# Performance work log

Hardware: AMD Instinct MI355X
Metric: run time of the kernel (lower is better)

The kernel has to match this reference:

```python
import jax, jax.numpy as jnp
import numpy as np

H = 12
D_MODEL = 768
H_D = D_MODEL // H


def setup_inputs() -> dict:
    key = jax.random.key(0)
    ks = jax.random.split(key, 11)
    B, S = 2, 2048
    scale_in = 1.0
    w_scale = 1.0 / np.sqrt(D_MODEL)
    inp = {
        "query": jax.random.normal(ks[0], (B, S, D_MODEL), dtype=jnp.float32),
        "key": jax.random.normal(ks[1], (B, S, D_MODEL), dtype=jnp.float32),
        "value": jax.random.normal(ks[2], (B, S, D_MODEL), dtype=jnp.float32),
        "wq": jax.random.normal(ks[3], (D_MODEL, D_MODEL), dtype=jnp.float32) * w_scale,
        "bq": jnp.zeros((D_MODEL,), dtype=jnp.float32),
        "wk": jax.random.normal(ks[4], (D_MODEL, D_MODEL), dtype=jnp.float32) * w_scale,
        "bk": jnp.zeros((D_MODEL,), dtype=jnp.float32),
        "wv": jax.random.normal(ks[5], (D_MODEL, D_MODEL), dtype=jnp.float32) * w_scale,
        "bv": jnp.zeros((D_MODEL,), dtype=jnp.float32),
        "wo": jax.random.normal(ks[6], (D_MODEL, D_MODEL), dtype=jnp.float32) * w_scale,
        "bo": jnp.zeros((D_MODEL,), dtype=jnp.float32),
    }
    return inp


def reference(query, key, value, wq, bq, wk, bk, wv, bv, wo, bo):
    B, S, _ = query.shape
    # QKV projections, split into heads: [B, H, S, h_d]
    def proj(x, w, b):
        y = jnp.einsum("bsd,de->bse", x, w) + b
        return y.reshape(B, S, H, H_D).transpose(0, 2, 1, 3)

    q = proj(query, wq, bq)
    k = proj(key, wk, bk)
    v = proj(value, wv, bv)

    # scaled dot-product attention (dropout disabled / eval mode)
    scores = jnp.einsum("bhsd,bhtd->bhst", q, k) / jnp.sqrt(jnp.float32(H_D))
    wm = jax.nn.softmax(scores, axis=-1)  # [B, H, S, S]
    out = jnp.einsum("bhst,bhtd->bhsd", wm, v)

    # merge heads and output projection
    out = out.transpose(0, 2, 1, 3).reshape(B, S, D_MODEL)
    out = jnp.einsum("bsd,de->bse", out, wo) + bo
    return out
```

## Files before the change

kernel.cpp:

```cpp
#include <hip/hip_runtime.h>

#define H 12
#define DM 768
#define HD 64
#define SEQ 2048
#define BATCH 2
#define MROWS (BATCH*SEQ)

typedef __attribute__((ext_vector_type(8))) short short8;
typedef __attribute__((ext_vector_type(4))) float f32x4;
typedef __attribute__((ext_vector_type(16))) float f32x16;
using u16 = unsigned short;
using u32 = unsigned int;

__device__ __forceinline__ float bf2f(u16 u) { return __uint_as_float(((u32)u) << 16); }
__device__ __forceinline__ u16 f2bf(float x) {
  u32 u = __float_as_uint(x);
  return (u16)((u + 0x7fffu + ((u >> 16) & 1u)) >> 16);
}
__device__ __forceinline__ u32 cvt_pk_bf16(float lo, float hi) {
  u32 r;
  asm("v_cvt_pk_bf16_f32 %0, %1, %2" : "=v"(r) : "v"(lo), "v"(hi));
  return r;
}
__device__ __forceinline__ void gl2lds16(const u16* __restrict__ g, u16* l) {
  __builtin_amdgcn_global_load_lds(
      (const __attribute__((address_space(1))) unsigned int*)g,
      (__attribute__((address_space(3))) unsigned int*)l,
      16, 0, 0);
}

#define C_SM 0.18033688011112042f

__global__ __launch_bounds__(256) void transpose_w4(const float* __restrict__ w0, const float* __restrict__ w1,
                                                    const float* __restrict__ w2, const float* __restrict__ w3,
                                                    u16* __restrict__ dst0)
{
  __shared__ u16 Ts[64][72];
  const float* src = blockIdx.z == 0 ? w0 : blockIdx.z == 1 ? w1 : blockIdx.z == 2 ? w2 : w3;
  u16* dst = dst0 + (size_t)blockIdx.z * DM * DM;
  const int t = threadIdx.x;
  const int r0 = blockIdx.y * 64, c0 = blockIdx.x * 64;
  const int row = t >> 2, cq = (t & 3) * 16;
  const float* sp = src + (size_t)(r0 + row) * DM + c0 + cq;
  #pragma unroll
  for (int g = 0; g < 4; ++g) {
    float4 a = *reinterpret_cast<const float4*>(sp + g * 4);
    Ts[row][cq + g * 4 + 0] = f2bf(a.x);
    Ts[row][cq + g * 4 + 1] = f2bf(a.y);
    Ts[row][cq + g * 4 + 2] = f2bf(a.z);
    Ts[row][cq + g * 4 + 3] = f2bf(a.w);
  }
  __syncthreads();
  union { uint4 v[2]; u16 e[16]; } pk;
  #pragma unroll
  for (int j = 0; j < 16; ++j) pk.e[j] = Ts[cq + j][row];
  uint4* dp = reinterpret_cast<uint4*>(dst + (size_t)(c0 + row) * DM + r0 + cq);
  dp[0] = pk.v[0];
  dp[1] = pk.v[1];
}

template<int BM, bool AF32>
__device__ __forceinline__ void gemm_core(const void* __restrict__ Av, const u16* __restrict__ Bt,
                                          const float* __restrict__ bias, void* __restrict__ dstv,
                                          int mode, int bx, int by, float outScale)
{
  constexpr int AFR = BM / 32;
  constexpr int ACH = BM / 32;
  __shared__ u16 As[BM * 64];
  __shared__ u16 Bs[128 * 64];
  const int t = threadIdx.x;
  const int lane = t & 63, w = t >> 6;
  const int l15 = lane & 15, l4 = lane >> 4;
  const int m0 = by * BM, n0 = bx * 128;
  const int wr = (w >> 1) * (BM / 2), wc = (w & 1) * 64;

  f32x4 acc[AFR][4] = {};

  for (int kt = 0; kt < DM / 64; ++kt) {
    const int k0 = kt * 64;
    #pragma unroll
    for (int c = 0; c < ACH; ++c) {
      const int id = c * 256 + t;
      const int row = id >> 3, xc = id & 7;
      const int db = row * 128 + ((xc * 16) ^ ((row & 7) << 4));
      if (AF32) {
        const float* Af = reinterpret_cast<const float*>(Av) + (size_t)(m0 + row) * DM + k0 + xc * 8;
        float4 a0 = *reinterpret_cast<const float4*>(Af);
        float4 a1 = *reinterpret_cast<const float4*>(Af + 4);
        uint4 v;
        v.x = cvt_pk_bf16(a0.x, a0.y);
        v.y = cvt_pk_bf16(a0.z, a0.w);
        v.z = cvt_pk_bf16(a1.x, a1.y);
        v.w = cvt_pk_bf16(a1.z, a1.w);
        *reinterpret_cast<uint4*>(reinterpret_cast<char*>(As) + db) = v;
      } else {
        uint4 va = *reinterpret_cast<const uint4*>(reinterpret_cast<const u16*>(Av) +
                   (size_t)(m0 + row) * DM + k0 + xc * 8);
        *reinterpret_cast<uint4*>(reinterpret_cast<char*>(As) + db) = va;
      }
    }
    #pragma unroll
    for (int c = 0; c < 4; ++c) {
      const int id = c * 256 + t;
      const int row = id >> 3, xc = id & 7;
      const int db = row * 128 + ((xc * 16) ^ ((row & 7) << 4));
      uint4 vb = *reinterpret_cast<const uint4*>(Bt + (size_t)(n0 + row) * DM + k0 + xc * 8);
      *reinterpret_cast<uint4*>(reinterpret_cast<char*>(Bs) + db) = vb;
    }
    __syncthreads();
    #pragma unroll
    for (int ks = 0; ks < 2; ++ks) {
      short8 ag[AFR], bg[4];
      #pragma unroll
      for (int i = 0; i < AFR; ++i) {
        const int ar = wr + i * 16 + l15;
        ag[i] = *reinterpret_cast<const short8*>(reinterpret_cast<const char*>(As) +
                 ar * 128 + ((ks * 64 + l4 * 16) ^ ((ar & 7) << 4)));
      }
      #pragma unroll
      for (int j = 0; j < 4; ++j) {
        const int br = wc + j * 16 + l15;
        bg[j] = *reinterpret_cast<const short8*>(reinterpret_cast<const char*>(Bs) +
                 br * 128 + ((ks * 64 + l4 * 16) ^ ((br & 7) << 4)));
      }
      #pragma unroll
      for (int i = 0; i < AFR; ++i)
        #pragma unroll
        for (int j = 0; j < 4; ++j)
          acc[i][j] = __builtin_amdgcn_mfma_f32_16x16x32_bf16(ag[i], bg[j], acc[i][j], 0, 0, 0);
    }
    __syncthreads();
  }

  #pragma unroll
  for (int j = 0; j < 4; ++j) {
    const int gcol = n0 + wc + j * 16 + l15;
    const float bb = bias[gcol];
    #pragma unroll
    for (int i = 0; i < AFR; ++i) {
      const int grow = m0 + wr + i * 16 + l4 * 4;
      if (mode == 2) {
        float* dst = reinterpret_cast<float*>(dstv);
        #pragma unroll
        for (int r = 0; r < 4; ++r)
          dst[(size_t)(grow + r) * DM + gcol] = acc[i][j][r] + bb;
      } else {
        u16* dst = reinterpret_cast<u16*>(dstv);
        const int b = grow >> 11, s = grow & (SEQ - 1);
        const int h = gcol >> 6, d = gcol & 63;
        if (mode == 0) {
          #pragma unroll
          for (int r = 0; r < 4; ++r)
            dst[((size_t)(b * H + h) * SEQ + s + r) * HD + d] = f2bf((acc[i][j][r] + bb) * outScale);
        } else {
          union { uint2 v; u16 e[4]; } pk;
          #pragma unroll
          for (int r = 0; r < 4; ++r) pk.e[r] = f2bf(acc[i][j][r] + bb);
          *reinterpret_cast<uint2*>(dst + ((size_t)(b * H + h) * HD + d) * SEQ + s) = pk.v;
        }
      }
    }
  }
}

__global__ __launch_bounds__(256) void gemm_qkv_kernel(
    const float* __restrict__ xq, const float* __restrict__ xk, const float* __restrict__ xv,
    const u16* __restrict__ wT, const float* __restrict__ bq, const float* __restrict__ bk,
    const float* __restrict__ bv, u16* __restrict__ Qb, u16* __restrict__ Kb, u16* __restrict__ Vtb)
{
  const int flat = blockIdx.z * 384 + blockIdx.y * 6 + blockIdx.x;
  const int nb = (flat & 7) * 144 + (flat >> 3);
  const int z = nb / 384, rem = nb % 384;
  const int by = rem / 6, bx = rem % 6;
  const float* A    = z == 0 ? xq : z == 1 ? xk : xv;
  const u16* Bt     = wT + (size_t)z * DM * DM;
  const float* bias = z == 0 ? bq : z == 1 ? bk : bv;
  u16* dst          = z == 0 ? Qb : z == 1 ? Kb : Vtb;
  const float sc    = z == 1 ? C_SM : 1.0f;
  gemm_core<64, true>(A, Bt, bias, dst, z == 2 ? 1 : 0, bx, by, sc);
}

__global__ __launch_bounds__(256) void gemm_o_kernel(const u16* __restrict__ A, const u16* __restrict__ woT,
                                                     const float* __restrict__ bo, float* __restrict__ out)
{
  const int flat = blockIdx.y * 6 + blockIdx.x;
  const int nb = (flat & 7) * 96 + (flat >> 3);
  gemm_core<32, false>(A, woT, bo, out, 2, nb % 6, nb / 6, 1.0f);
}

__global__ __launch_bounds__(256) void attn_kernel(const u16* __restrict__ Q, const u16* __restrict__ K,
                                                   const u16* __restrict__ Vt, u16* __restrict__ attn)
{
  __shared__ u16 Ks[2][64 * 64];
  __shared__ u16 Vs[2][64 * 64];
  __shared__ u16 Qs[128 * 64];
  const int t = threadIdx.x;
  const int lane = t & 63, w = t >> 6;
  const int l31 = lane & 31, hi = lane >> 5;
  const int flat = blockIdx.y * 16 + blockIdx.x;
  const int nbid = (flat & 7) * 48 + (flat >> 3);
  const int q0 = (nbid & 15) * 128;
  const int bh = nbid >> 4;
  const size_t qbase  = ((size_t)bh * SEQ + q0) * HD;
  const size_t kbase0 = (size_t)bh * SEQ * HD;
  const size_t vtbase = (size_t)bh * HD * SEQ;

  const int r8 = lane >> 3;
  const int pcol = ((lane & 7) ^ r8) * 8;

  #pragma unroll
  for (int j = 0; j < 4; ++j) {
    const int ci = w * 4 + j;
    gl2lds16(Q + qbase + (size_t)(ci * 8 + r8) * HD + pcol, &Qs[ci * 512]);
  }
  #pragma unroll
  for (int j = 0; j < 2; ++j) {
    const int ci = w * 2 + j;
    const int row = ci * 8 + r8;
    gl2lds16(K + kbase0 + (size_t)row * HD + pcol, &Ks[0][ci * 512]);
    gl2lds16(Vt + vtbase + (size_t)row * SEQ + pcol, &Vs[0][ci * 512]);
  }
  asm volatile("s_waitcnt vmcnt(4)" ::: "memory");

  short8 qf[4];
  {
    const int qr = w * 32 + l31;
    #pragma unroll
    for (int ks = 0; ks < 4; ++ks)
      qf[ks] = *reinterpret_cast<const short8*>(reinterpret_cast<const char*>(Qs) +
               qr * 128 + (((ks * 32 + hi * 16)) ^ ((qr & 7) << 4)));
  }

  f32x16 oacc[2] = {};
  float l_s = 0.f;
  int cur = 0;

  for (int kt = 0; kt < SEQ / 64; ++kt) {
    asm volatile("s_waitcnt vmcnt(0)" ::: "memory");
    __builtin_amdgcn_s_barrier();

    if (kt + 1 < SEQ / 64) {
      const int nxt = cur ^ 1;
      #pragma unroll
      for (int j = 0; j < 2; ++j) {
        const int ci = w * 2 + j;
        const int row = ci * 8 + r8;
        gl2lds16(K + kbase0 + (size_t)((kt + 1) * 64 + row) * HD + pcol, &Ks[nxt][ci * 512]);
        gl2lds16(Vt + vtbase + (size_t)row * SEQ + (kt + 1) * 64 + pcol, &Vs[nxt][ci * 512]);
      }
    }

    f32x16 s0 = {}, s1 = {};
    __builtin_amdgcn_s_setprio(1);
    #pragma unroll
    for (int ks = 0; ks < 4; ++ks) {
      const int cb = ks * 32 + hi * 16;
      short8 kf0 = *reinterpret_cast<const short8*>(reinterpret_cast<const char*>(Ks[cur]) +
                   l31 * 128 + (cb ^ ((l31 & 7) << 4)));
      short8 kf1 = *reinterpret_cast<const short8*>(reinterpret_cast<const char*>(Ks[cur]) +
                   (32 + l31) * 128 + (cb ^ ((l31 & 7) << 4)));
      s0 = __builtin_amdgcn_mfma_f32_32x32x16_bf16(kf0, qf[ks], s0, 0, 0, 0);
      s1 = __builtin_amdgcn_mfma_f32_32x32x16_bf16(kf1, qf[ks], s1, 0, 0, 0);
    }
    __builtin_amdgcn_s_setprio(0);

    float p0[16], p1[16], psum = 0.f;
    #pragma unroll
    for (int r = 0; r < 16; ++r) {
      p0[r] = exp2f(s0[r]);
      p1[r] = exp2f(s1[r]);
      psum += p0[r] + p1[r];
    }
    l_s += psum;

    __builtin_amdgcn_s_setprio(1);
    #pragma unroll
    for (int ks2 = 0; ks2 < 4; ++ks2) {
      const float* P = (ks2 < 2) ? p0 : p1;
      const int ro = (ks2 & 1) * 8;
      u32 a0 = cvt_pk_bf16(P[ro + 0], P[ro + 1]);
      u32 a1 = cvt_pk_bf16(P[ro + 2], P[ro + 3]);
      u32 b0 = cvt_pk_bf16(P[ro + 4], P[ro + 5]);
      u32 b1 = cvt_pk_bf16(P[ro + 6], P[ro + 7]);
      asm volatile("v_permlane32_swap_b32 %0, %1" : "+v"(a0), "+v"(b0));
      asm volatile("v_permlane32_swap_b32 %0, %1" : "+v"(a1), "+v"(b1));
      union { u32 u[4]; short8 s; } pa;
      pa.u[0] = a0; pa.u[1] = a1; pa.u[2] = b0; pa.u[3] = b1;
      const int cb2 = ks2 * 32 + hi * 16;
      #pragma unroll
      for (int dt = 0; dt < 2; ++dt) {
        const int vr = dt * 32 + l31;
        short8 vf = *reinterpret_cast<const short8*>(reinterpret_cast<const char*>(Vs[cur]) +
                    vr * 128 + (cb2 ^ ((vr & 7) << 4)));
        oacc[dt] = __builtin_amdgcn_mfma_f32_32x32x16_bf16(pa.s, vf, oacc[dt], 0, 0, 0);
      }
    }
    __builtin_amdgcn_s_setprio(0);
    cur ^= 1;
  }

  const float l_tot = l_s + __shfl_xor(l_s, 32);
  const int b = bh / H, h = bh % H;
  #pragma unroll
  for (int r = 0; r < 16; ++r) {
    const int qo = (r & 3) + 8 * (r >> 2) + 4 * hi;
    const float inv = 1.f / __shfl(l_tot, qo);
    const int qg = q0 + w * 32 + qo;
    const size_t base = ((size_t)(b * SEQ + qg)) * DM + h * HD;
    attn[base + l31]      = f2bf(oacc[0][r] * inv);
    attn[base + 32 + l31] = f2bf(oacc[1][r] * inv);
  }
}

extern "C" void kernel_launch(void* const* d_in, const int* in_sizes, int n_in,
                              void* d_out, int out_size, void* d_ws, size_t ws_size,
                              hipStream_t stream)
{
  const float* q  = (const float*)d_in[0];
  const float* k  = (const float*)d_in[1];
  const float* v  = (const float*)d_in[2];
  const float* wq = (const float*)d_in[3];
  const float* bq = (const float*)d_in[4];
  const float* wk = (const float*)d_in[5];
  const float* bk = (const float*)d_in[6];
  const float* wv = (const float*)d_in[7];
  const float* bv = (const float*)d_in[8];
  const float* wo = (const float*)d_in[9];
  const float* bo = (const float*)d_in[10];

  u16* ws = (u16*)d_ws;
  const size_t WSZ = (size_t)DM * DM;
  const size_t TSZ = (size_t)MROWS * DM;
  u16* wT  = ws;
  u16* Qb  = ws + 4 * WSZ;
  u16* Kb  = Qb + TSZ;
  u16* Vtb = Kb + TSZ;
  u16* Ab  = Vtb + TSZ;

  transpose_w4<<<dim3(12, 12, 4), 256, 0, stream>>>(wq, wk, wv, wo, wT);
  gemm_qkv_kernel<<<dim3(6, 64, 3), 256, 0, stream>>>(q, k, v, wT, bq, bk, bv, Qb, Kb, Vtb);
  attn_kernel<<<dim3(16, BATCH * H), 256, 0, stream>>>(Qb, Kb, Vtb, Ab);
  gemm_o_kernel<<<dim3(6, 128), 256, 0, stream>>>(Ab, wT + 3 * WSZ, bo, (float*)d_out);
}
```

Measured before the change: 116.5 us.

## Split attention over two KV halves and merge partial outputs in separate kernel

Each attention block now processes only half of the key/value sequence, doubling the grid to spread work across more CUs and reduce wave-quantization tail. Unnormalized fp32 partial outputs and row sums are written to workspace, and a new merge kernel sums the halves, normalizes, converts to bf16 and writes the head-merged layout. Q fragments are loaded directly from global memory instead of staging through LDS. This adds extra global traffic for fp32 partials and an additional kernel launch.

```diff
diff --git a/kernel.cpp b/kernel.cpp
--- a/kernel.cpp
+++ b/kernel.cpp
@@ -190,64 +190,63 @@
 }
 
 __global__ __launch_bounds__(256) void attn_kernel(const u16* __restrict__ Q, const u16* __restrict__ K,
-                                                   const u16* __restrict__ Vt, u16* __restrict__ attn)
+                                                   const u16* __restrict__ Vt,
+                                                   float* __restrict__ Op0, float* __restrict__ Op1,
+                                                   float* __restrict__ Lp0, float* __restrict__ Lp1)
 {
   __shared__ u16 Ks[2][64 * 64];
   __shared__ u16 Vs[2][64 * 64];
-  __shared__ u16 Qs[128 * 64];
   const int t = threadIdx.x;
   const int lane = t & 63, w = t >> 6;
   const int l31 = lane & 31, hi = lane >> 5;
-  const int flat = blockIdx.y * 16 + blockIdx.x;
-  const int nbid = (flat & 7) * 48 + (flat >> 3);
-  const int q0 = (nbid & 15) * 128;
-  const int bh = nbid >> 4;
+  const int flat = blockIdx.y * 32 + blockIdx.x;
+  const int nbid = (flat & 7) * 96 + (flat >> 3);
+  const int bh = nbid >> 5;
+  const int rem = nbid & 31;
+  const int q0 = (rem >> 1) * 128;
+  const int half = rem & 1;
+  const int kv0 = half * (SEQ / 2);
   const size_t qbase  = ((size_t)bh * SEQ + q0) * HD;
   const size_t kbase0 = (size_t)bh * SEQ * HD;
   const size_t vtbase = (size_t)bh * HD * SEQ;
+  float* __restrict__ Op = half ? Op1 : Op0;
+  float* __restrict__ Lp = half ? Lp1 : Lp0;
 
   const int r8 = lane >> 3;
   const int pcol = ((lane & 7) ^ r8) * 8;
 
-  #pragma unroll
-  for (int j = 0; j < 4; ++j) {
-    const int ci = w * 4 + j;
-    gl2lds16(Q + qbase + (size_t)(ci * 8 + r8) * HD + pcol, &Qs[ci * 512]);
-  }
+  short8 qf[4];
+  {
+    const u16* qp = Q + qbase + (size_t)(w * 32 + l31) * HD + hi * 8;
+    #pragma unroll
+    for (int ks = 0; ks < 4; ++ks)
+      qf[ks] = *reinterpret_cast<const short8*>(qp + ks * 16);
+  }
+
   #pragma unroll
   for (int j = 0; j < 2; ++j) {
     const int ci = w * 2 + j;
     const int row = ci * 8 + r8;
-    gl2lds16(K + kbase0 + (size_t)row * HD + pcol, &Ks[0][ci * 512]);
-    gl2lds16(Vt + vtbase + (size_t)row * SEQ + pcol, &Vs[0][ci * 512]);
-  }
-  asm volatile("s_waitcnt vmcnt(4)" ::: "memory");
-
-  short8 qf[4];
-  {
-    const int qr = w * 32 + l31;
-    #pragma unroll
-    for (int ks = 0; ks < 4; ++ks)
-      qf[ks] = *reinterpret_cast<const short8*>(reinterpret_cast<const char*>(Qs) +
-               qr * 128 + (((ks * 32 + hi * 16)) ^ ((qr & 7) << 4)));
+    gl2lds16(K + kbase0 + (size_t)(kv0 + row) * HD + pcol, &Ks[0][ci * 512]);
+    gl2lds16(Vt + vtbase + (size_t)row * SEQ + kv0 + pcol, &Vs[0][ci * 512]);
   }
 
   f32x16 oacc[2] = {};
   float l_s = 0.f;
   int cur = 0;
 
-  for (int kt = 0; kt < SEQ / 64; ++kt) {
+  for (int kt = 0; kt < SEQ / 2 / 64; ++kt) {
     asm volatile("s_waitcnt vmcnt(0)" ::: "memory");
     __builtin_amdgcn_s_barrier();
 
-    if (kt + 1 < SEQ / 64) {
+    if (kt + 1 < SEQ / 2 / 64) {
       const int nxt = cur ^ 1;
       #pragma unroll
       for (int j = 0; j < 2; ++j) {
         const int ci = w * 2 + j;
         const int row = ci * 8 + r8;
-        gl2lds16(K + kbase0 + (size_t)((kt + 1) * 64 + row) * HD + pcol, &Ks[nxt][ci * 512]);
-        gl2lds16(Vt + vtbase + (size_t)row * SEQ + (kt + 1) * 64 + pcol, &Vs[nxt][ci * 512]);
+        gl2lds16(K + kbase0 + (size_t)(kv0 + (kt + 1) * 64 + row) * HD + pcol, &Ks[nxt][ci * 512]);
+        gl2lds16(Vt + vtbase + (size_t)row * SEQ + kv0 + (kt + 1) * 64 + pcol, &Vs[nxt][ci * 512]);
       }
     }
 
@@ -301,16 +300,32 @@
   }
 
   const float l_tot = l_s + __shfl_xor(l_s, 32);
-  const int b = bh / H, h = bh % H;
+  if (hi == 0)
+    Lp[(size_t)bh * SEQ + q0 + w * 32 + l31] = l_tot;
   #pragma unroll
   for (int r = 0; r < 16; ++r) {
     const int qo = (r & 3) + 8 * (r >> 2) + 4 * hi;
-    const float inv = 1.f / __shfl(l_tot, qo);
-    const int qg = q0 + w * 32 + qo;
-    const size_t base = ((size_t)(b * SEQ + qg)) * DM + h * HD;
-    attn[base + l31]      = f2bf(oacc[0][r] * inv);
-    attn[base + 32 + l31] = f2bf(oacc[1][r] * inv);
-  }
+    const size_t base = ((size_t)bh * SEQ + q0 + w * 32 + qo) * HD;
+    Op[base + l31]      = oacc[0][r];
+    Op[base + 32 + l31] = oacc[1][r];
+  }
+}
+
+__global__ __launch_bounds__(256) void attn_merge(const float* __restrict__ Op0, const float* __restrict__ Op1,
+                                                  const float* __restrict__ Lp0, const float* __restrict__ Lp1,
+                                                  u16* __restrict__ Ab)
+{
+  const int id = blockIdx.x * 256 + threadIdx.x;
+  const int row = id >> 4, dc = (id & 15) * 4;
+  const int bh = row >> 11, q = row & (SEQ - 1);
+  const int b = bh / H, h = bh % H;
+  const float inv = 1.f / (Lp0[row] + Lp1[row]);
+  float4 o0 = *reinterpret_cast<const float4*>(Op0 + (size_t)row * HD + dc);
+  float4 o1 = *reinterpret_cast<const float4*>(Op1 + (size_t)row * HD + dc);
+  uint2 o;
+  o.x = cvt_pk_bf16((o0.x + o1.x) * inv, (o0.y + o1.y) * inv);
+  o.y = cvt_pk_bf16((o0.z + o1.z) * inv, (o0.w + o1.w) * inv);
+  *reinterpret_cast<uint2*>(Ab + ((size_t)(b * SEQ + q)) * DM + h * HD + dc) = o;
 }
 
 extern "C" void kernel_launch(void* const* d_in, const int* in_sizes, int n_in,
@@ -332,14 +347,20 @@
   u16* ws = (u16*)d_ws;
   const size_t WSZ = (size_t)DM * DM;
   const size_t TSZ = (size_t)MROWS * DM;
+  const size_t NQ  = (size_t)BATCH * H * SEQ;
   u16* wT  = ws;
   u16* Qb  = ws + 4 * WSZ;
   u16* Kb  = Qb + TSZ;
   u16* Vtb = Kb + TSZ;
   u16* Ab  = Vtb + TSZ;
+  float* Op0 = (float*)(Ab + TSZ);
+  float* Op1 = Op0 + TSZ;
+  float* Lp0 = Op1 + TSZ;
+  float* Lp1 = Lp0 + NQ;
 
   transpose_w4<<<dim3(12, 12, 4), 256, 0, stream>>>(wq, wk, wv, wo, wT);
   gemm_qkv_kernel<<<dim3(6, 64, 3), 256, 0, stream>>>(q, k, v, wT, bq, bk, bv, Qb, Kb, Vtb);
-  attn_kernel<<<dim3(16, BATCH * H), 256, 0, stream>>>(Qb, Kb, Vtb, Ab);
+  attn_kernel<<<dim3(32, 24), 256, 0, stream>>>(Qb, Kb, Vtb, Op0, Op1, Lp0, Lp1);
+  attn_merge<<<dim3((int)(NQ * 16 / 256)), 256, 0, stream>>>(Op0, Op1, Lp0, Lp1, Ab);
   gemm_o_kernel<<<dim3(6, 128), 256, 0, stream>>>(Ab, wT + 3 * WSZ, bo, (float*)d_out);
 }
```

Result: no change. 117.9 us (+1.1%).
